# Performance work log

Measured on AMD Instinct MI355X. Metric: run time of the kernel, lower is better.

## Reference

```python
import jax, jax.numpy as jnp
import numpy as np

NUM_GRAPHS = 256
N_NODES = 100000
N_EDGES = 1200000
NODE_DIM = 64
NUM_LAYERS = 3
R_HID = 128
R_OUT = 32


def setup_inputs() -> dict:
    key = jax.random.key(0)
    ks = jax.random.split(key, 10)
    x = jax.random.normal(ks[0], (N_NODES, NODE_DIM), dtype=jnp.float32)
    src = jax.random.randint(ks[1], (N_EDGES,), 0, N_NODES)
    dst = jax.random.randint(ks[2], (N_EDGES,), 0, N_NODES)
    graph_ids = jnp.sort(jax.random.randint(ks[3], (N_NODES,), 0, NUM_GRAPHS))
    s = 1.0 / np.sqrt(NODE_DIM)
    gin_W = jax.random.normal(ks[4], (NUM_LAYERS, NODE_DIM, NODE_DIM), dtype=jnp.float32) * s
    gin_b = jnp.zeros((NUM_LAYERS, NODE_DIM), dtype=jnp.float32)
    eps = jnp.zeros((NUM_LAYERS,), dtype=jnp.float32)  # learnable GIN epsilon
    in_dim = NODE_DIM * NUM_LAYERS
    r_W1 = jax.random.normal(ks[5], (in_dim, R_HID), dtype=jnp.float32) / np.sqrt(in_dim)
    r_b1 = jnp.zeros((R_HID,), dtype=jnp.float32)
    r_W2 = jax.random.normal(ks[6], (R_HID, R_OUT), dtype=jnp.float32) / np.sqrt(R_HID)
    r_b2 = jnp.zeros((R_OUT,), dtype=jnp.float32)
    return {"x": x, "gin_W": gin_W, "gin_b": gin_b, "eps": eps,
            "r_W1": r_W1, "r_b1": r_b1, "r_W2": r_W2, "r_b2": r_b2,
            "src": src, "dst": dst, "graph_ids": graph_ids}


def reference(x, gin_W, gin_b, eps, r_W1, r_b1, r_W2, r_b2, src, dst, graph_ids):
    n = x.shape[0]
    h = x
    hs = []
    for l in range(NUM_LAYERS):  # fixed small layer loop
        # neighbor sum aggregation: scatter-add messages h[src] into dst
        agg = jax.ops.segment_sum(h[src], dst, num_segments=n)  # [N, D]
        h = jax.nn.relu(((1.0 + eps[l]) * h + agg) @ gin_W[l] + gin_b[l])
        hs.append(h)
    H = jnp.stack(hs, axis=1)  # [N, L, D]
    # dgl.sum_nodes per layer output == ragged segment-sum over graph ids
    g = jax.ops.segment_sum(H, graph_ids, num_segments=NUM_GRAPHS)  # [B, L, D]
    g = g.reshape(NUM_GRAPHS, -1)  # [B, L*D]
    # readout MLP (2 layers)
    out = jax.nn.relu(g @ r_W1 + r_b1) @ r_W2 + r_b2
    return out
```

## Files before the change

### kernel.cpp

```cpp
#include <hip/hip_runtime.h>


#define NBLK 512
#define BS 512
#define CAPSH 13

typedef unsigned short ushort_t;
typedef __bf16 v8bf __attribute__((ext_vector_type(8)));
typedef float v4f __attribute__((ext_vector_type(4)));

__device__ __forceinline__ float h2f_lo(unsigned int v) {
    return (float)__builtin_bit_cast(_Float16, (unsigned short)(v & 0xffffu));
}
__device__ __forceinline__ float h2f_hi(unsigned int v) {
    return (float)__builtin_bit_cast(_Float16, (unsigned short)(v >> 16));
}
__device__ __forceinline__ unsigned int f2h(float f) {
    return (unsigned int)__builtin_bit_cast(unsigned short, (_Float16)f);
}

__global__ __launch_bounds__(256) void scatter_pre_kernel(
        const int* __restrict__ src, const int* __restrict__ dst,
        int* __restrict__ cnt, unsigned int* __restrict__ bkt,
        int E, int nbkt, int ebpb,
        const float* __restrict__ x, ushort_t* __restrict__ xh, int n4, int castBlocks,
        const float* __restrict__ W, ushort_t* __restrict__ whi,
        ushort_t* __restrict__ wlo, int wtotal) {
    __shared__ int lcnt[256];
    __shared__ int lbase[256];
    __shared__ int lrank[256];
    int t = threadIdx.x;
    int blk = blockIdx.x;
    if (blk < NBLK) {
        lcnt[t] = 0; lrank[t] = 0;
        __syncthreads();
        int base = blk * ebpb;
        int end = min(base + ebpb, E);
        for (int i = base + t; i < end; i += 256)
            atomicAdd(&lcnt[dst[i] >> 9], 1);
        __syncthreads();
        if (t < nbkt && lcnt[t])
            lbase[t] = (t << CAPSH) + atomicAdd(&cnt[t], lcnt[t]);
        __syncthreads();
        for (int i = base + t; i < end; i += 256) {
            int d = dst[i];
            int b = d >> 9;
            int r = atomicAdd(&lrank[b], 1);
            bkt[lbase[b] + r] = ((unsigned int)src[i] << 9) | (unsigned int)(d & (BS - 1));
        }
    } else if (blk < NBLK + castBlocks) {
        int i = (blk - NBLK) * 256 + t;
        if (i < n4) {
            float4 v = ((const float4*)x)[i];
            uint2 p;
            p.x = f2h(v.x) | (f2h(v.y) << 16);
            p.y = f2h(v.z) | (f2h(v.w) << 16);
            ((uint2*)xh)[i] = p;
        }
    } else {
        int i = (blk - NBLK - castBlocks) * 256 + t;
        if (i < wtotal) {
            int l = i >> 12, r = i & 4095;
            int n = r >> 6, k = r & 63;
            float w = W[l * 4096 + k * 64 + n];
            __bf16 h = (__bf16)w;
            float rem = w - (float)h;
            whi[i] = __builtin_bit_cast(ushort_t, h);
            wlo[i] = __builtin_bit_cast(ushort_t, (__bf16)rem);
        }
    }
}

__global__ __launch_bounds__(256) void csr_build_kernel(
        const unsigned int* __restrict__ bkt, const int* __restrict__ cnt,
        int* __restrict__ offsets, int* __restrict__ csr, int N, int nbkt) {
    __shared__ int c0[BS];
    __shared__ int rk[BS];
    __shared__ int sh[256];
    int b = blockIdx.x, t = threadIdx.x;
    int v = (t < nbkt) ? cnt[t] : 0;
    sh[t] = v;
    __syncthreads();
    for (int off = 1; off < 256; off <<= 1) {
        int u = (t >= off) ? sh[t - off] : 0;
        __syncthreads();
        sh[t] += u;
        __syncthreads();
    }
    int gbase = (b == 0) ? 0 : sh[b - 1];
    int cb = cnt[b];
    __syncthreads();
    c0[t] = 0; c0[t + 256] = 0;
    rk[t] = 0; rk[t + 256] = 0;
    __syncthreads();
    int sbase = b << CAPSH;
    for (int i = t; i < cb; i += 256)
        atomicAdd(&c0[bkt[sbase + i] & (BS - 1)], 1);
    __syncthreads();
    int i0 = 2 * t, i1 = 2 * t + 1;
    int v0 = c0[i0], v1 = c0[i1];
    int pair = v0 + v1;
    sh[t] = pair;
    __syncthreads();
    for (int off = 1; off < 256; off <<= 1) {
        int u = (t >= off) ? sh[t - off] : 0;
        __syncthreads();
        sh[t] += u;
        __syncthreads();
    }
    int ex = sh[t] - pair;
    __syncthreads();
    c0[i0] = ex;
    c0[i1] = ex + v0;
    __syncthreads();
    int d0 = (b << 9) + i0;
    if (d0 <= N) offsets[d0] = gbase + c0[i0];
    int d1 = (b << 9) + i1;
    if (d1 <= N) offsets[d1] = gbase + c0[i1];
    for (int i = t; i < cb; i += 256) {
        unsigned int vv = bkt[sbase + i];
        int dl = vv & (BS - 1);
        int r = atomicAdd(&rk[dl], 1);
        csr[gbase + c0[dl] + r] = (int)(vv >> 9);
    }
}

#define CONSUME_NODE(kk, dgv, e0v, buf, sf) { \
    float ax = 0.f, ay = 0.f, az = 0.f, aw = 0.f; \
    _Pragma("unroll") \
    for (int j = 0; j < 6; ++j) { \
        if (g + 4 * j < (dgv)) { \
            ax += h2f_lo(buf[j].x); ay += h2f_hi(buf[j].x); \
            az += h2f_lo(buf[j].y); aw += h2f_hi(buf[j].y); } } \
    if ((dgv) > 24) {                    \
        int dc_ = min((dgv), 64); \
        for (int j = 24 + g; j < dc_; j += 4) { \
            int s_ = __shfl(idxa[kk], j, 64); \
            uint2 v_ = hp2[(size_t)s_ * 16 + sl]; \
            ax += h2f_lo(v_.x); ay += h2f_hi(v_.x); \
            az += h2f_lo(v_.y); aw += h2f_hi(v_.y); } \
        for (int j = 64 + g; j < (dgv); j += 4) {    \
            int s_ = csr[(e0v) + j]; \
            uint2 v_ = hp2[(size_t)s_ * 16 + sl]; \
            ax += h2f_lo(v_.x); ay += h2f_hi(v_.x); \
            az += h2f_lo(v_.y); aw += h2f_hi(v_.y); } } \
    ax += __shfl_xor(ax, 16, 64); ax += __shfl_xor(ax, 32, 64); \
    ay += __shfl_xor(ay, 16, 64); ay += __shfl_xor(ay, 32, 64); \
    az += __shfl_xor(az, 16, 64); az += __shfl_xor(az, 32, 64); \
    aw += __shfl_xor(aw, 16, 64); aw += __shfl_xor(aw, 32, 64); \
    if (tile * 16 + (kk) < N) { \
        ax = fmaf(eps1, h2f_lo(sf.x), ax); ay = fmaf(eps1, h2f_hi(sf.x), ay); \
        az = fmaf(eps1, h2f_lo(sf.y), az); aw = fmaf(eps1, h2f_hi(sf.y), aw); } \
    if (g == 0) { \
        float4 r4_; r4_.x = ax; r4_.y = ay; r4_.z = az; r4_.w = aw; \
        *(float4*)&myrows[(kk) * 64 + sl * 4] = r4_; } }

__global__ __launch_bounds__(256, 4) void layer_kernel(
        const ushort_t* __restrict__ hin, ushort_t* __restrict__ hout,
        const int* __restrict__ offsets, const int* __restrict__ csr,
        const ushort_t* __restrict__ wt_hi, const ushort_t* __restrict__ wt_lo,
        const float* __restrict__ gin_b, const float* __restrict__ eps_arr,
        int layer, int N, int E) {
    __shared__ float rows[4 * 16 * 64];
    int t = threadIdx.x;
    int wv = t >> 6, lane = t & 63;
    int tile = blockIdx.x * 4 + wv;
    if (tile * 16 >= N) return;
    float* myrows = rows + wv * 16 * 64;
    const uint2* hp2 = (const uint2*)hin;
    float eps1 = 1.0f + eps_arr[layer];

    int g  = lane >> 4;
    int sl = lane & 15;

    int off_l = offsets[min(tile * 16 + lane, N)];
    int e0a[17];
    #pragma unroll
    for (int k = 0; k < 17; ++k)
        e0a[k] = __builtin_amdgcn_readlane(off_l, k);

    int idxa[16];
    #pragma unroll
    for (int k = 0; k < 16; ++k) {
        int dg_ = e0a[k + 1] - e0a[k];
        int v_ = csr[min(e0a[k] + lane, E - 1)];
        idxa[k] = (lane < dg_) ? v_ : 0;
    }

    #pragma unroll
    for (int kb = 0; kb < 8; ++kb) {
        const int k = kb * 2;
        int e0A = e0a[k],     dgA = e0a[k + 1] - e0a[k];
        int e0B = e0a[k + 1], dgB = e0a[k + 2] - e0a[k + 1];
        uint2 b[6], c[6];
        #pragma unroll
        for (int j = 0; j < 6; ++j) {
            int p = g + 4 * j;
            int s = (p < dgA) ? __shfl(idxa[k], p, 64) : 0;
            b[j] = hp2[(size_t)s * 16 + sl];
        }
        #pragma unroll
        for (int j = 0; j < 6; ++j) {
            int p = g + 4 * j;
            int s = (p < dgB) ? __shfl(idxa[k + 1], p, 64) : 0;
            c[j] = hp2[(size_t)s * 16 + sl];
        }
        uint2 sfA = hp2[(size_t)min(tile * 16 + k,     N - 1) * 16 + sl];
        uint2 sfB = hp2[(size_t)min(tile * 16 + k + 1, N - 1) * 16 + sl];
        __builtin_amdgcn_sched_barrier(0);
        CONSUME_NODE(k,     dgA, e0A, b, sfA)
        CONSUME_NODE(k + 1, dgB, e0B, c, sfB)
    }

    int c2 = lane & 15;
    int q  = lane >> 4;
    int node16 = tile * 16 + c2;

    const ushort_t* Whi = wt_hi + layer * 4096;
    const ushort_t* Wlo = wt_lo + layer * 4096;
    const float*    bl  = gin_b + layer * 64;

    v8bf bhi[2], blo2[2];
    #pragma unroll
    for (int kt = 0; kt < 2; ++kt) {
        float4 f0 = *(float4*)&myrows[c2 * 64 + kt * 32 + q * 8];
        float4 f1 = *(float4*)&myrows[c2 * 64 + kt * 32 + q * 8 + 4];
        float xs[8] = {f0.x, f0.y, f0.z, f0.w, f1.x, f1.y, f1.z, f1.w};
        #pragma unroll
        for (int j = 0; j < 8; ++j) {
            __bf16 h = (__bf16)xs[j];
            bhi[kt][j] = h;
            blo2[kt][j] = (__bf16)(xs[j] - (float)h);
        }
    }

    #pragma unroll
    for (int mt = 0; mt < 4; ++mt) {
        v4f acc = {0.f, 0.f, 0.f, 0.f};
        #pragma unroll
        for (int kt = 0; kt < 2; ++kt) {
            int dim = mt * 16 + c2;
            size_t off = (size_t)dim * 64 + kt * 32 + q * 8;
            v8bf ah = __builtin_bit_cast(v8bf, *(const uint4*)(Whi + off));
            v8bf al = __builtin_bit_cast(v8bf, *(const uint4*)(Wlo + off));
            acc = __builtin_amdgcn_mfma_f32_16x16x32_bf16(ah, bhi[kt],  acc, 0, 0, 0);
            acc = __builtin_amdgcn_mfma_f32_16x16x32_bf16(ah, blo2[kt], acc, 0, 0, 0);
            acc = __builtin_amdgcn_mfma_f32_16x16x32_bf16(al, bhi[kt],  acc, 0, 0, 0);
        }
        float4 bv = ((const float4*)(bl + mt * 16))[q];
        float o0 = fmaxf(acc[0] + bv.x, 0.f);
        float o1 = fmaxf(acc[1] + bv.y, 0.f);
        float o2 = fmaxf(acc[2] + bv.z, 0.f);
        float o3 = fmaxf(acc[3] + bv.w, 0.f);
        uint2 pk;
        pk.x = f2h(o0) | (f2h(o1) << 16);
        pk.y = f2h(o2) | (f2h(o3) << 16);
        if (node16 < N)
            *(uint2*)(hout + (size_t)node16 * 64 + mt * 16 + q * 4) = pk;
    }
}

__global__ __launch_bounds__(384) void readout_mlp_kernel(
        const ushort_t* __restrict__ H, const int* __restrict__ gids,
        const float* __restrict__ W1, const float* __restrict__ b1,
        const float* __restrict__ W2, const float* __restrict__ b2,
        float* __restrict__ out, int N) {
    __shared__ float part[6][64];
    __shared__ float gr[192];
    __shared__ float hid[128];
    int graph = blockIdx.x;
    int t = threadIdx.x;
    int w = t >> 6, lane = t & 63;
    int l = w >> 1, p = w & 1;
    int lo = 0, hi = N;
    while (lo < hi) { int m = (lo + hi) >> 1; if (gids[m] < graph) lo = m + 1; else hi = m; }
    int start = lo;
    int lo2 = start, hi2 = N;
    while (lo2 < hi2) { int m = (lo2 + hi2) >> 1; if (gids[m] < graph + 1) lo2 = m + 1; else hi2 = m; }
    int end = lo2;
    int nd  = lane >> 4;
    int slp = lane & 15;
    float a0 = 0.f, a1 = 0.f, a2 = 0.f, a3 = 0.f;
    const uint2* Hl = (const uint2*)(H + (size_t)l * N * 64);
    for (int n = start + p * 4 + nd; n < end; n += 8) {
        uint2 v = Hl[(size_t)n * 16 + slp];
        a0 += h2f_lo(v.x); a1 += h2f_hi(v.x);
        a2 += h2f_lo(v.y); a3 += h2f_hi(v.y);
    }
    a0 += __shfl_xor(a0, 16, 64); a0 += __shfl_xor(a0, 32, 64);
    a1 += __shfl_xor(a1, 16, 64); a1 += __shfl_xor(a1, 32, 64);
    a2 += __shfl_xor(a2, 16, 64); a2 += __shfl_xor(a2, 32, 64);
    a3 += __shfl_xor(a3, 16, 64); a3 += __shfl_xor(a3, 32, 64);
    if (lane < 16) {
        float4 r4; r4.x = a0; r4.y = a1; r4.z = a2; r4.w = a3;
        *(float4*)&part[w][slp * 4] = r4;
    }
    __syncthreads();
    if (t < 192) {
        int ll = t >> 6, d = t & 63;
        gr[t] = part[ll * 2][d] + part[ll * 2 + 1][d];
    }
    __syncthreads();
    if (t < 128) {
        float s = b1[t];
        for (int k = 0; k < 192; ++k) s = fmaf(gr[k], W1[k * 128 + t], s);
        hid[t] = fmaxf(s, 0.0f);
    }
    __syncthreads();
    if (t < 32) {
        float s = b2[t];
        for (int k = 0; k < 128; ++k) s = fmaf(hid[k], W2[k * 32 + t], s);
        out[graph * 32 + t] = s;
    }
}

extern "C" void kernel_launch(void* const* d_in, const int* in_sizes, int n_in,
                              void* d_out, int out_size, void* d_ws, size_t ws_size,
                              hipStream_t stream) {
    const float* x     = (const float*)d_in[0];
    const float* gin_W = (const float*)d_in[1];
    const float* gin_b = (const float*)d_in[2];
    const float* eps   = (const float*)d_in[3];
    const float* r_W1  = (const float*)d_in[4];
    const float* r_b1  = (const float*)d_in[5];
    const float* r_W2  = (const float*)d_in[6];
    const float* r_b2  = (const float*)d_in[7];
    const int*   src   = (const int*)d_in[8];
    const int*   dst   = (const int*)d_in[9];
    const int*   gids  = (const int*)d_in[10];

    int N = in_sizes[0] / 64;
    int E = in_sizes[8];
    int B = out_size / 32;

    int nbkt = (N + BS - 1) / BS;
    int ebpb = (E + NBLK - 1) / NBLK;
    int n4 = N * 64 / 4;
    int castBlocks = (n4 + 255) / 256;
    int wtotal = 3 * 4096;
    int prepBlocks = (wtotal + 255) / 256;
    int bktTot = nbkt << CAPSH;

    int* ws       = (int*)d_ws;
    int* cnt      = ws;
    int* offsets  = cnt + nbkt;
    unsigned int* bkt = (unsigned int*)(offsets + (N + 1));
    int* csr      = (int*)(bkt + bktTot);
    size_t w      = (size_t)(csr + E - ws);
    w = (w + 15) & ~(size_t)15;
    ushort_t* xh  = (ushort_t*)(ws + w);
    ushort_t* H   = xh + (size_t)N * 64;
    ushort_t* whi = H + 3 * (size_t)N * 64;
    ushort_t* wlo = whi + 3 * 4096;

    hipMemsetAsync(cnt, 0, nbkt * sizeof(int), stream);
    scatter_pre_kernel<<<NBLK + castBlocks + prepBlocks, 256, 0, stream>>>(
        src, dst, cnt, bkt, E, nbkt, ebpb,
        x, xh, n4, castBlocks, gin_W, whi, wlo, wtotal);
    csr_build_kernel<<<nbkt, 256, 0, stream>>>(bkt, cnt, offsets, csr, N, nbkt);

    int lbk = (N + 63) / 64;
    ushort_t* H0 = H;
    ushort_t* H1 = H + (size_t)N * 64;
    ushort_t* H2 = H + 2 * (size_t)N * 64;

    layer_kernel<<<lbk, 256, 0, stream>>>(xh, H0, offsets, csr, whi, wlo, gin_b, eps, 0, N, E);
    layer_kernel<<<lbk, 256, 0, stream>>>(H0, H1, offsets, csr, whi, wlo, gin_b, eps, 1, N, E);
    layer_kernel<<<lbk, 256, 0, stream>>>(H1, H2, offsets, csr, whi, wlo, gin_b, eps, 2, N, E);

    readout_mlp_kernel<<<B, 384, 0, stream>>>(H, gids, r_W1, r_b1, r_W2, r_b2, (float*)d_out, N);
}
```

Before: 298.5 us.

## Stage bucket and CSR scatter writes in shared memory for coalesced global stores

Result: no change. 299.9 us (+0.5%).

```diff
diff --git a/kernel.cpp b/kernel.cpp
--- a/kernel.cpp
+++ b/kernel.cpp
@@ -1,7 +1,8 @@
 #include <hip/hip_runtime.h>
 
 
-#define NBLK 512
+#define SBLK 256
+#define EBPB_MAX 4704
 #define BS 512
 #define CAPSH 13
 
@@ -26,12 +27,15 @@
         const float* __restrict__ x, ushort_t* __restrict__ xh, int n4, int castBlocks,
         const float* __restrict__ W, ushort_t* __restrict__ whi,
         ushort_t* __restrict__ wlo, int wtotal) {
+    __shared__ unsigned int staged[EBPB_MAX];
+    __shared__ unsigned char bidA[EBPB_MAX];
     __shared__ int lcnt[256];
+    __shared__ int lofs[256];
+    __shared__ int lrank[256];
     __shared__ int lbase[256];
-    __shared__ int lrank[256];
     int t = threadIdx.x;
     int blk = blockIdx.x;
-    if (blk < NBLK) {
+    if (blk < SBLK) {
         lcnt[t] = 0; lrank[t] = 0;
         __syncthreads();
         int base = blk * ebpb;
@@ -39,17 +43,36 @@
         for (int i = base + t; i < end; i += 256)
             atomicAdd(&lcnt[dst[i] >> 9], 1);
         __syncthreads();
-        if (t < nbkt && lcnt[t])
-            lbase[t] = (t << CAPSH) + atomicAdd(&cnt[t], lcnt[t]);
+        int v = lcnt[t];
+        lofs[t] = v;
+        __syncthreads();
+        for (int off = 1; off < 256; off <<= 1) {
+            int u = (t >= off) ? lofs[t - off] : 0;
+            __syncthreads();
+            lofs[t] += u;
+            __syncthreads();
+        }
+        int ex = lofs[t] - v;
+        __syncthreads();
+        lofs[t] = ex;
+        if (t < nbkt && v) lbase[t] = (t << CAPSH) + atomicAdd(&cnt[t], v);
         __syncthreads();
         for (int i = base + t; i < end; i += 256) {
             int d = dst[i];
             int b = d >> 9;
             int r = atomicAdd(&lrank[b], 1);
-            bkt[lbase[b] + r] = ((unsigned int)src[i] << 9) | (unsigned int)(d & (BS - 1));
-        }
-    } else if (blk < NBLK + castBlocks) {
-        int i = (blk - NBLK) * 256 + t;
+            int j = lofs[b] + r;
+            staged[j] = ((unsigned int)src[i] << 9) | (unsigned int)(d & (BS - 1));
+            bidA[j] = (unsigned char)b;
+        }
+        __syncthreads();
+        int tot = end - base;
+        for (int j = t; j < tot; j += 256) {
+            int b = bidA[j];
+            bkt[lbase[b] + (j - lofs[b])] = staged[j];
+        }
+    } else if (blk < SBLK + castBlocks) {
+        int i = (blk - SBLK) * 256 + t;
         if (i < n4) {
             float4 v = ((const float4*)x)[i];
             uint2 p;
@@ -58,7 +81,7 @@
             ((uint2*)xh)[i] = p;
         }
     } else {
-        int i = (blk - NBLK - castBlocks) * 256 + t;
+        int i = (blk - SBLK - castBlocks) * 256 + t;
         if (i < wtotal) {
             int l = i >> 12, r = i & 4095;
             int n = r >> 6, k = r & 63;
@@ -74,6 +97,7 @@
 __global__ __launch_bounds__(256) void csr_build_kernel(
         const unsigned int* __restrict__ bkt, const int* __restrict__ cnt,
         int* __restrict__ offsets, int* __restrict__ csr, int N, int nbkt) {
+    __shared__ unsigned int stagedE[1 << CAPSH];
     __shared__ int c0[BS];
     __shared__ int rk[BS];
     __shared__ int sh[256];
@@ -121,8 +145,11 @@
         unsigned int vv = bkt[sbase + i];
         int dl = vv & (BS - 1);
         int r = atomicAdd(&rk[dl], 1);
-        csr[gbase + c0[dl] + r] = (int)(vv >> 9);
-    }
+        stagedE[c0[dl] + r] = vv >> 9;
+    }
+    __syncthreads();
+    for (int j = t; j < cb; j += 256)
+        csr[gbase + j] = (int)stagedE[j];
 }
 
 #define CONSUME_NODE(kk, dgv, e0v, buf, sf) { \
@@ -334,7 +361,7 @@
     int B = out_size / 32;
 
     int nbkt = (N + BS - 1) / BS;
-    int ebpb = (E + NBLK - 1) / NBLK;
+    int ebpb = (E + SBLK - 1) / SBLK;
     int n4 = N * 64 / 4;
     int castBlocks = (n4 + 255) / 256;
     int wtotal = 3 * 4096;
@@ -354,7 +381,7 @@
     ushort_t* wlo = whi + 3 * 4096;
 
     hipMemsetAsync(cnt, 0, nbkt * sizeof(int), stream);
-    scatter_pre_kernel<<<NBLK + castBlocks + prepBlocks, 256, 0, stream>>>(
+    scatter_pre_kernel<<<SBLK + castBlocks + prepBlocks, 256, 0, stream>>>(
         src, dst, cnt, bkt, E, nbkt, ebpb,
         x, xh, n4, castBlocks, gin_W, whi, wlo, wtotal);
     csr_build_kernel<<<nbkt, 256, 0, stream>>>(bkt, cnt, offsets, csr, N, nbkt);
```
